# Kernel optimization log

Measured on AMD Instinct MI355X. Metric: run time of the kernel, lower is better.

## Reference

```python
import jax, jax.numpy as jnp
import numpy as np

H = 16        # num_attention_heads
G = 16        # groups
SCALE_MIN = 0.95
SCALE_MAX = 1.05


def setup_inputs() -> dict:
    key = jax.random.key(0)
    ks = jax.random.split(key, 9)
    B, S, E = 2, 2048, 1024
    d = {
        'hidden_states': jax.random.normal(ks[0], (B, S, E), jnp.float32),
        'Wq': jax.random.normal(ks[1], (E, E), jnp.float32) * (E ** -0.5),
        'bq': jax.random.normal(ks[2], (E,), jnp.float32) * 0.02,
        'Wk': jax.random.normal(ks[3], (E, E), jnp.float32) * (E ** -0.5),
        'bk': jax.random.normal(ks[4], (E,), jnp.float32) * 0.02,
        'Wv': jax.random.normal(ks[5], (E, E), jnp.float32) * (E ** -0.5),
        'bv': jax.random.normal(ks[6], (E,), jnp.float32) * 0.02,
        'Ws': jax.random.normal(ks[7], (H * G, E), jnp.float32) * (E ** -0.5),
        'bs': jax.random.normal(ks[8], (H * G,), jnp.float32) * 0.02,
    }
    return d


def _shape_heads(x, B, S):
    # [B,S,h*D] -> [B,h,S,D]
    return x.reshape(B, S, H, -1).transpose(0, 2, 1, 3)


def reference(hidden_states, Wq, bq, Wk, bk, Wv, bv, Ws, bs):
    B, S, E = hidden_states.shape
    D = E // H            # head dim = 64
    gd = D // G           # group dim = 4

    Q = _shape_heads(hidden_states @ Wq.T + bq, B, S)   # [B,h,S,D]
    K = _shape_heads(hidden_states @ Wk.T + bk, B, S)
    V = _shape_heads(hidden_states @ Wv.T + bv, B, S)

    # groupwise dynamic scales, narrow sigmoid range
    s_logits = hidden_states @ Ws.T + bs                 # [B,S,h*g]
    s = jax.nn.sigmoid(s_logits) * (SCALE_MAX - SCALE_MIN) + SCALE_MIN
    s = s.reshape(B, S, H, G).transpose(0, 2, 1, 3)      # [B,h,S,g]
    s = jnp.repeat(s, gd, axis=-1)                       # [B,h,S,D]

    Q = Q * s  # apply_to='q'

    scores = jnp.einsum('bhsd,bhtd->bhst', Q, K) / jnp.sqrt(jnp.float32(D))
    probs = jax.nn.softmax(scores, axis=-1)
    ctx = jnp.einsum('bhst,bhtd->bhsd', probs, V)        # [B,h,S,D]
    ctx = ctx.transpose(0, 2, 1, 3).reshape(B, S, H * D)
    return ctx
```

## Files before the change

kernel.cpp:

```cpp
#include <hip/hip_runtime.h>

typedef short bf16x8 __attribute__((ext_vector_type(8)));
typedef short bf16x4 __attribute__((ext_vector_type(4)));
typedef float f32x4 __attribute__((ext_vector_type(4)));

__device__ inline float bf2f(ushort u) {
    unsigned v = ((unsigned)u) << 16;
    return __builtin_bit_cast(float, v);
}
__device__ inline ushort f2bf(float f) {
    unsigned u = __builtin_bit_cast(unsigned, f);
    u += 0x7fffu + ((u >> 16) & 1u);
    return (ushort)(u >> 16);
}
__device__ inline void async_load16(const ushort* g, ushort* l) {
    __builtin_amdgcn_global_load_lds((const __attribute__((address_space(1))) void*)g,
                                     (__attribute__((address_space(3))) void*)l, 16, 0, 0);
}
__device__ inline f32x4 mfma16(bf16x4 a, bf16x4 b, f32x4 c) {
#if __has_builtin(__builtin_amdgcn_mfma_f32_16x16x16_bf16)
    return __builtin_amdgcn_mfma_f32_16x16x16_bf16(a, b, c, 0, 0, 0);
#else
    return __builtin_amdgcn_mfma_f32_16x16x16bf16_1k(a, b, c, 0, 0, 0);
#endif
}

__global__ void cast_all(const float* __restrict__ hs, const float* __restrict__ Wq,
                         const float* __restrict__ Wk, const float* __restrict__ Wv,
                         const float* __restrict__ Ws,
                         ushort* __restrict__ dhs, ushort* __restrict__ dWq,
                         ushort* __restrict__ dWk, ushort* __restrict__ dWv,
                         ushort* __restrict__ dWs)
{
    int bid = blockIdx.x;
    const float* src; ushort* dst; int off;
    if (bid < 2048)      { src = hs; dst = dhs; off = bid; }
    else if (bid < 2560) { src = Wq; dst = dWq; off = bid - 2048; }
    else if (bid < 3072) { src = Wk; dst = dWk; off = bid - 2560; }
    else if (bid < 3584) { src = Wv; dst = dWv; off = bid - 3072; }
    else                 { src = Ws; dst = dWs; off = bid - 3584; }
    int i = (off * 256 + threadIdx.x) * 8;
    float4 a = *(const float4*)(src + i);
    float4 b = *(const float4*)(src + i + 4);
    union { ushort u[8]; float4 v; } o;
    o.u[0] = f2bf(a.x); o.u[1] = f2bf(a.y); o.u[2] = f2bf(a.z); o.u[3] = f2bf(a.w);
    o.u[4] = f2bf(b.x); o.u[5] = f2bf(b.y); o.u[6] = f2bf(b.z); o.u[7] = f2bf(b.w);
    *(float4*)(dst + i) = o.v;
}

__launch_bounds__(256, 4)
__global__ void fused_qkvs(const ushort* __restrict__ X,
                           const ushort* __restrict__ Wq, const ushort* __restrict__ Wk,
                           const ushort* __restrict__ Wv, const ushort* __restrict__ Ws,
                           const float* __restrict__ bq, const float* __restrict__ bk,
                           const float* __restrict__ bv, const float* __restrict__ bs,
                           ushort* __restrict__ Qb, ushort* __restrict__ Kb,
                           ushort* __restrict__ VtG, float* __restrict__ sb)
{
    __shared__ __align__(16) ushort Sm[128 * 136];
    ushort* As = Sm;
    ushort* Bs = Sm + 128 * 64;

    const int tid = threadIdx.x, w = tid >> 6, lane = tid & 63;
    const int l15 = lane & 15, quad = lane >> 4;
    const int lrow = lane >> 3;
    const int gchunk = ((lane & 7) ^ lrow) * 8;

    const int wid = blockIdx.x;
    const int r8 = wid & 7, jj = wid >> 3;
    const int by = (jj & 3) * 8 + r8;
    const int xb = jj >> 2;
    const int m0 = by * 128;

    const ushort* W; const float* bias; int n0, mode;
    if (xb < 8)       { W = Wq; bias = bq; n0 = xb * 128;        mode = 1; }
    else if (xb < 16) { W = Wk; bias = bk; n0 = (xb - 8) * 128;  mode = 0; }
    else if (xb < 24) { W = Wv; bias = bv; n0 = (xb - 16) * 128; mode = 2; }
    else              { W = Ws; bias = bs; n0 = (xb - 24) * 128; mode = 3; }

    const int wm = (w >> 1) * 64, wn = (w & 1) * 64;

    f32x4 acc[4][4];
    for (int i = 0; i < 4; i++) for (int j = 0; j < 4; j++) acc[i][j] = (f32x4){0.f, 0.f, 0.f, 0.f};

    for (int k0 = 0; k0 < 1024; k0 += 64) {
        __syncthreads();
        for (int c = 0; c < 4; ++c) {
            int r = w * 32 + c * 8;
            async_load16(&X[(size_t)(m0 + r + lrow) * 1024 + k0 + gchunk], &As[r * 64]);
            async_load16(&W[(size_t)(n0 + r + lrow) * 1024 + k0 + gchunk], &Bs[r * 64]);
        }
        __syncthreads();
        for (int kk = 0; kk < 64; kk += 32) {
            const int csw = quad + (kk >> 3);
            bf16x8 a[4], b[4];
            for (int i = 0; i < 4; i++)
                a[i] = *(const bf16x8*)&As[(wm + i * 16 + l15) * 64 + ((csw ^ (l15 & 7)) * 8)];
            for (int j = 0; j < 4; j++)
                b[j] = *(const bf16x8*)&Bs[(wn + j * 16 + l15) * 64 + ((csw ^ (l15 & 7)) * 8)];
            for (int i = 0; i < 4; i++)
                for (int j = 0; j < 4; j++)
                    acc[i][j] = __builtin_amdgcn_mfma_f32_16x16x32_bf16(a[i], b[j], acc[i][j], 0, 0, 0);
        }
    }

    const float QSCALE = 0.125f * 1.44269504f;

    if (mode == 3) {
        for (int i = 0; i < 4; i++)
            for (int j = 0; j < 4; j++) {
                int gn = n0 + wn + j * 16 + l15;
                float bv_ = bias[gn];
                for (int r = 0; r < 4; r++) {
                    int gm = m0 + wm + i * 16 + quad * 4 + r;
                    float v = acc[i][j][r] + bv_;
                    float sg = __builtin_amdgcn_rcpf(1.0f + __builtin_amdgcn_exp2f(-v * 1.44269504f));
                    sb[(size_t)gm * 256 + gn] = sg * 0.1f + 0.95f;
                }
            }
        return;
    }

    __syncthreads();

    if (mode == 2) {
        for (int i = 0; i < 4; i++)
            for (int j = 0; j < 4; j++) {
                int gnl = wn + j * 16 + l15;
                float bv_ = bias[n0 + gnl];
                ushort4 pk;
                pk.x = f2bf(acc[i][j][0] + bv_);
                pk.y = f2bf(acc[i][j][1] + bv_);
                pk.z = f2bf(acc[i][j][2] + bv_);
                pk.w = f2bf(acc[i][j][3] + bv_);
                *(ushort4*)&Sm[gnl * 136 + wm + i * 16 + quad * 4] = pk;
            }
        __syncthreads();
        const int bb = m0 >> 11, sloc = m0 & 2047;
        for (int it = 0; it < 8; ++it) {
            int d = (tid >> 4) + it * 16;
            int s8 = (tid & 15) * 8;
            float4 v = *(float4*)&Sm[d * 136 + s8];
            int h = (n0 + d) >> 6, dd = d & 63;
            *(float4*)&VtG[(size_t)(bb * 16 + h) * 131072 + (size_t)dd * 2048 + sloc + s8] = v;
        }
    } else {
        for (int i = 0; i < 4; i++)
            for (int j = 0; j < 4; j++) {
                int gnl = wn + j * 16 + l15;
                float bv_ = bias[n0 + gnl];
                for (int r = 0; r < 4; r++) {
                    float v = acc[i][j][r] + bv_;
                    if (mode == 1) v *= QSCALE;
                    Sm[(wm + i * 16 + quad * 4 + r) * 136 + gnl] = f2bf(v);
                }
            }
        __syncthreads();
        ushort* dst = (mode == 1) ? Qb : Kb;
        for (int it = 0; it < 8; ++it) {
            int row = (tid >> 4) + it * 16, c = (tid & 15) * 8;
            *(float4*)&dst[(size_t)(m0 + row) * 1024 + n0 + c] = *(float4*)&Sm[row * 136 + c];
        }
    }
}

__launch_bounds__(256, 2)
__global__ void attn_kernel(const ushort* __restrict__ Q, const ushort* __restrict__ K,
                            const ushort* __restrict__ Vt, const float* __restrict__ sb,
                            float* __restrict__ out)
{
    __shared__ __align__(16) ushort SmA[4 * 4096 + 8192];
    ushort* Ks0 = SmA;
    ushort* Ks1 = SmA + 4096;
    ushort* Vs0 = SmA + 8192;
    ushort* Vs1 = SmA + 12288;
    ushort* Qs  = SmA + 16384;

    const int tid = threadIdx.x, w = tid >> 6, lane = tid & 63;
    const int l15 = lane & 15, quad = lane >> 4;
    const int lrow = lane >> 3;
    const int gchunk = ((lane & 7) ^ lrow) * 8;

    const int wid = blockIdx.x;
    const int r8 = wid & 7, jj = wid >> 3;
    const int bh = (jj & 3) * 8 + r8;
    const int qx = jj >> 2;
    const int b = bh >> 4, h = bh & 15;
    const int q0 = qx * 128;
    const size_t rowbase = (size_t)b * 2048;
    const int cbase = h * 64;

    const ushort* kg = K + (rowbase + w * 16 + lrow) * 1024 + cbase + gchunk;
    const ushort* vg = Vt + (size_t)bh * 131072 + (size_t)(w * 16 + lrow) * 2048 + gchunk;

    for (int c = 0; c < 2; ++c) {
        async_load16(kg + c * 8192,  Ks0 + w * 1024 + c * 512);
        async_load16(vg + c * 16384, Vs0 + w * 1024 + c * 512);
    }

    for (int it = 0; it < 4; ++it) {
        int l = tid + it * 256;
        int r = l >> 3, ch = l & 7;
        int c = ch * 8;
        union { float4 f; ushort u[8]; } uu, oo;
        uu.f = *(const float4*)&Q[(rowbase + q0 + r) * 1024 + cbase + c];
        const float* sp = &sb[(rowbase + q0 + r) * 256 + ((cbase + c) >> 2)];
        float s0 = sp[0], s1 = sp[1];
        for (int j = 0; j < 4; j++) oo.u[j] = f2bf(bf2f(uu.u[j]) * s0);
        for (int j = 4; j < 8; j++) oo.u[j] = f2bf(bf2f(uu.u[j]) * s1);
        *(float4*)&Qs[r * 64 + ((ch ^ (r & 7)) * 8)] = oo.f;
    }
    __syncthreads();

    bf16x8 aq[2][2];
    for (int mt = 0; mt < 2; mt++)
        for (int kk2 = 0; kk2 < 2; kk2++)
            aq[mt][kk2] = *(const bf16x8*)&Qs[(w * 32 + mt * 16 + l15) * 64
                                              + (((kk2 * 4 + quad) ^ (l15 & 7)) * 8)];

    int kvoff[2][4];
    for (int kk2 = 0; kk2 < 2; kk2++)
        for (int nt = 0; nt < 4; nt++)
            kvoff[kk2][nt] = (nt * 16 + l15) * 64 + (((quad + kk2 * 4) ^ (l15 & 7)) * 8);
    int vaddr[4];
    for (int kt2 = 0; kt2 < 4; kt2++)
        vaddr[kt2] = l15 * 64 + (quad & 1) * 4
                   + (((kt2 * 2 + (quad >> 1)) ^ (l15 & 7)) * 8);

    const bf16x4 vones4 = {0x3F80, 0x3F80, 0x3F80, 0x3F80};

    f32x4 osum[2];
    f32x4 o[2][4];
    for (int mt = 0; mt < 2; mt++) {
        osum[mt] = (f32x4){0.f, 0.f, 0.f, 0.f};
        for (int nt = 0; nt < 4; nt++) o[mt][nt] = (f32x4){0.f, 0.f, 0.f, 0.f};
    }
    const f32x4 z4 = (f32x4){0.f, 0.f, 0.f, 0.f};

#define ATTN_STEP(KC, VC, KN, VN, KT, PREFETCH)                                                         \
    {                                                                                                   \
        __syncthreads();                  \
        if (PREFETCH) {                                                                                 \
            const int nk = (KT) + 1;                                                                    \
            for (int c = 0; c < 2; ++c) {                                                               \
                async_load16(kg + nk * 65536 + c * 8192, KN + w * 1024 + c * 512);                      \
                async_load16(vg + nk * 64 + c * 16384,   VN + w * 1024 + c * 512);                      \
            }                                                                                           \
        }                                                                                               \
        bf16x8 kb[2][4];                                                                                \
        for (int kk2 = 0; kk2 < 2; kk2++)                                                               \
            for (int nt = 0; nt < 4; nt++)                                                              \
                kb[kk2][nt] = *(const bf16x8*)&KC[kvoff[kk2][nt]];                                      \
        bf16x4 vb4[4][4];                                                                               \
        _Pragma("unroll")                                                                               \
        for (int kt2 = 0; kt2 < 4; kt2++)                                                               \
            _Pragma("unroll")                                                                           \
            for (int nt = 0; nt < 4; nt++)                                                              \
                vb4[kt2][nt] = *(const bf16x4*)&VC[vaddr[kt2] + nt * 1024];                             \
        _Pragma("unroll")                                                                               \
        for (int mt = 0; mt < 2; mt++) {                                                                \
                                                     \
            f32x4 st[4];                                                                                \
            _Pragma("unroll")                                                                           \
            for (int kt2 = 0; kt2 < 4; kt2++) {                                                         \
                st[kt2] = __builtin_amdgcn_mfma_f32_16x16x32_bf16(kb[0][kt2], aq[mt][0], z4, 0, 0, 0);  \
                st[kt2] = __builtin_amdgcn_mfma_f32_16x16x32_bf16(kb[1][kt2], aq[mt][1], st[kt2],       \
                                                                  0, 0, 0);                             \
            }                                                                                           \
                           \
            unsigned du0[4], du1[4];                                                                    \
            _Pragma("unroll")                                                                           \
            for (int kt2 = 0; kt2 < 4; kt2++) {                                                         \
                float p0 = __builtin_amdgcn_exp2f(st[kt2][0]);                                          \
                float p1 = __builtin_amdgcn_exp2f(st[kt2][1]);                                          \
                float p2 = __builtin_amdgcn_exp2f(st[kt2][2]);                                          \
                float p3 = __builtin_amdgcn_exp2f(st[kt2][3]);                                          \
                du0[kt2] = __builtin_amdgcn_perm(__builtin_bit_cast(unsigned, p1) + 0x8000u,            \
                                                 __builtin_bit_cast(unsigned, p0) + 0x8000u,            \
                                                 0x07060302u);                                          \
                du1[kt2] = __builtin_amdgcn_perm(__builtin_bit_cast(unsigned, p3) + 0x8000u,            \
                                                 __builtin_bit_cast(unsigned, p2) + 0x8000u,            \
                                                 0x07060302u);                                          \
            }                                                                                           \
                              \
            _Pragma("unroll")                                                                           \
            for (int kt2 = 0; kt2 < 4; kt2++) {                                                         \
                union { unsigned u[2]; bf16x4 v; } af;                                                  \
                af.u[0] = du0[kt2]; af.u[1] = du1[kt2];                                                 \
                osum[mt] = mfma16(af.v, vones4, osum[mt]);                                              \
                _Pragma("unroll")                                                                       \
                for (int nt = 0; nt < 4; nt++)                                                          \
                    o[mt][nt] = mfma16(af.v, vb4[kt2][nt], o[mt][nt]);                                  \
            }                                                                                           \
        }                                                                                               \
    }

    for (int kt = 0; kt < 32; kt += 2) {
        ATTN_STEP(Ks0, Vs0, Ks1, Vs1, kt, 1);
        ATTN_STEP(Ks1, Vs1, Ks0, Vs0, kt + 1, (kt + 2 < 32));
    }
#undef ATTN_STEP

    for (int mt = 0; mt < 2; mt++) {
        for (int r = 0; r < 4; r++) {
            float iv = __builtin_amdgcn_rcpf(osum[mt][r]);
            int q = q0 + w * 32 + mt * 16 + quad * 4 + r;
            size_t base = (rowbase + q) * 1024 + cbase;
            for (int nt = 0; nt < 4; nt++)
                out[base + nt * 16 + l15] = o[mt][nt][r] * iv;
        }
    }
}

extern "C" void kernel_launch(void* const* d_in, const int* in_sizes, int n_in,
                              void* d_out, int out_size, void* d_ws, size_t ws_size,
                              hipStream_t stream) {
    const float* hs = (const float*)d_in[0];
    const float* Wq = (const float*)d_in[1];
    const float* bq = (const float*)d_in[2];
    const float* Wk = (const float*)d_in[3];
    const float* bk = (const float*)d_in[4];
    const float* Wv = (const float*)d_in[5];
    const float* bv = (const float*)d_in[6];
    const float* Ws = (const float*)d_in[7];
    const float* bs = (const float*)d_in[8];
    float* outp = (float*)d_out;

    char* ws = (char*)d_ws;
    ushort* Qb    = (ushort*)(ws);
    ushort* Kb    = (ushort*)(ws + 8388608);
    ushort* VtG   = (ushort*)(ws + 16777216);
    float*  sb    = (float* )(ws + 25165824);
    ushort* hs_bf = (ushort*)(ws + 29360128);
    ushort* Wq_bf = (ushort*)(ws + 37748736);
    ushort* Wk_bf = (ushort*)(ws + 39845888);
    ushort* Wv_bf = (ushort*)(ws + 41943040);
    ushort* Ws_bf = (ushort*)(ws + 44040192);

    cast_all<<<dim3(3712), dim3(256), 0, stream>>>(hs, Wq, Wk, Wv, Ws,
                                                   hs_bf, Wq_bf, Wk_bf, Wv_bf, Ws_bf);
    fused_qkvs<<<dim3(832), dim3(256), 0, stream>>>(hs_bf, Wq_bf, Wk_bf, Wv_bf, Ws_bf,
                                                    bq, bk, bv, bs, Qb, Kb, VtG, sb);
    attn_kernel<<<dim3(512), dim3(256), 0, stream>>>(Qb, Kb, VtG, sb, outp);
}
```

Before: 169.3 us.

## Double KV tile size per barrier and load scaled Q directly to registers

```diff
diff --git a/kernel.cpp b/kernel.cpp
--- a/kernel.cpp
+++ b/kernel.cpp
@@ -169,12 +169,11 @@
                             const ushort* __restrict__ Vt, const float* __restrict__ sb,
                             float* __restrict__ out)
 {
-    __shared__ __align__(16) ushort SmA[4 * 4096 + 8192];
+    __shared__ __align__(16) ushort SmA[4 * 8192];
     ushort* Ks0 = SmA;
-    ushort* Ks1 = SmA + 4096;
-    ushort* Vs0 = SmA + 8192;
-    ushort* Vs1 = SmA + 12288;
-    ushort* Qs  = SmA + 16384;
+    ushort* Ks1 = SmA + 8192;
+    ushort* Vs0 = SmA + 16384;
+    ushort* Vs1 = SmA + 24576;
 
     const int tid = threadIdx.x, w = tid >> 6, lane = tid & 63;
     const int l15 = lane & 15, quad = lane >> 4;
@@ -190,33 +189,29 @@
     const size_t rowbase = (size_t)b * 2048;
     const int cbase = h * 64;
 
-    const ushort* kg = K + (rowbase + w * 16 + lrow) * 1024 + cbase + gchunk;
+    const ushort* kg = K + (rowbase + w * 32 + lrow) * 1024 + cbase + gchunk;
     const ushort* vg = Vt + (size_t)bh * 131072 + (size_t)(w * 16 + lrow) * 2048 + gchunk;
 
-    for (int c = 0; c < 2; ++c) {
-        async_load16(kg + c * 8192,  Ks0 + w * 1024 + c * 512);
-        async_load16(vg + c * 16384, Vs0 + w * 1024 + c * 512);
-    }
-
-    for (int it = 0; it < 4; ++it) {
-        int l = tid + it * 256;
-        int r = l >> 3, ch = l & 7;
-        int c = ch * 8;
-        union { float4 f; ushort u[8]; } uu, oo;
-        uu.f = *(const float4*)&Q[(rowbase + q0 + r) * 1024 + cbase + c];
-        const float* sp = &sb[(rowbase + q0 + r) * 256 + ((cbase + c) >> 2)];
-        float s0 = sp[0], s1 = sp[1];
-        for (int j = 0; j < 4; j++) oo.u[j] = f2bf(bf2f(uu.u[j]) * s0);
-        for (int j = 4; j < 8; j++) oo.u[j] = f2bf(bf2f(uu.u[j]) * s1);
-        *(float4*)&Qs[r * 64 + ((ch ^ (r & 7)) * 8)] = oo.f;
-    }
-    __syncthreads();
+    for (int c = 0; c < 4; ++c)
+        async_load16(kg + c * 8192, Ks0 + w * 2048 + c * 512);
+    for (int ss = 0; ss < 2; ++ss)
+        for (int c = 0; c < 2; ++c)
+            async_load16(vg + ss * 64 + c * 16384, Vs0 + ss * 4096 + w * 1024 + c * 512);
 
     bf16x8 aq[2][2];
     for (int mt = 0; mt < 2; mt++)
-        for (int kk2 = 0; kk2 < 2; kk2++)
-            aq[mt][kk2] = *(const bf16x8*)&Qs[(w * 32 + mt * 16 + l15) * 64
-                                              + (((kk2 * 4 + quad) ^ (l15 & 7)) * 8)];
+        for (int kk2 = 0; kk2 < 2; kk2++) {
+            size_t qrow = rowbase + q0 + w * 32 + mt * 16 + l15;
+            int c0 = cbase + kk2 * 32 + quad * 8;
+            union { float4 f; ushort u[8]; } uu;
+            union { ushort u[8]; bf16x8 v; } oo;
+            uu.f = *(const float4*)&Q[qrow * 1024 + c0];
+            const float* sp = &sb[qrow * 256 + (c0 >> 2)];
+            float s0 = sp[0], s1 = sp[1];
+            for (int j = 0; j < 4; j++) oo.u[j] = f2bf(bf2f(uu.u[j]) * s0);
+            for (int j = 4; j < 8; j++) oo.u[j] = f2bf(bf2f(uu.u[j]) * s1);
+            aq[mt][kk2] = oo.v;
+        }
 
     int kvoff[2][4];
     for (int kk2 = 0; kk2 < 2; kk2++)
@@ -242,62 +237,70 @@
         __syncthreads();                  \
         if (PREFETCH) {                                                                                 \
             const int nk = (KT) + 1;                                                                    \
-            for (int c = 0; c < 2; ++c) {                                                               \
-                async_load16(kg + nk * 65536 + c * 8192, KN + w * 1024 + c * 512);                      \
-                async_load16(vg + nk * 64 + c * 16384,   VN + w * 1024 + c * 512);                      \
+            for (int c = 0; c < 4; ++c)                                                                 \
+                async_load16(kg + (size_t)nk * 131072 + c * 8192, KN + w * 2048 + c * 512);             \
+            for (int ss = 0; ss < 2; ++ss)                                                              \
+                for (int c = 0; c < 2; ++c)                                                             \
+                    async_load16(vg + nk * 128 + ss * 64 + c * 16384,                                   \
+                                 VN + ss * 4096 + w * 1024 + c * 512);                                  \
+        }                                                                                               \
+        _Pragma("unroll")                                                                               \
+        for (int sub = 0; sub < 2; ++sub) {                                                             \
+            const ushort* KCs = KC + sub * 4096;                                                        \
+            const ushort* VCs = VC + sub * 4096;                                                        \
+            bf16x8 kb[2][4];                                                                            \
+            for (int kk2 = 0; kk2 < 2; kk2++)                                                           \
+                for (int nt = 0; nt < 4; nt++)                                                          \
+                    kb[kk2][nt] = *(const bf16x8*)&KCs[kvoff[kk2][nt]];                                 \
+            bf16x4 vb4[4][4];                                                                           \
+            _Pragma("unroll")                                                                           \
+            for (int kt2 = 0; kt2 < 4; kt2++)                                                           \
+                _Pragma("unroll")                                                                       \
+                for (int nt = 0; nt < 4; nt++)                                                          \
+                    vb4[kt2][nt] = *(const bf16x4*)&VCs[vaddr[kt2] + nt * 1024];                        \
+            _Pragma("unroll")                                                                           \
+            for (int mt = 0; mt < 2; mt++) {                                                            \
+                                                     \
+                f32x4 st[4];                                                                            \
+                _Pragma("unroll")                                                                       \
+                for (int kt2 = 0; kt2 < 4; kt2++) {                                                     \
+                    st[kt2] = __builtin_amdgcn_mfma_f32_16x16x32_bf16(kb[0][kt2], aq[mt][0],            \
+                                                                      z4, 0, 0, 0);                     \
+                    st[kt2] = __builtin_amdgcn_mfma_f32_16x16x32_bf16(kb[1][kt2], aq[mt][1],            \
+                                                                      st[kt2], 0, 0, 0);                \
+                }                                                                                       \
+                           \
+                unsigned du0[4], du1[4];                                                                \
+                _Pragma("unroll")                                                                       \
+                for (int kt2 = 0; kt2 < 4; kt2++) {                                                     \
+                    float p0 = __builtin_amdgcn_exp2f(st[kt2][0]);                                      \
+                    float p1 = __builtin_amdgcn_exp2f(st[kt2][1]);                                      \
+                    float p2 = __builtin_amdgcn_exp2f(st[kt2][2]);                                      \
+                    float p3 = __builtin_amdgcn_exp2f(st[kt2][3]);                                      \
+                    du0[kt2] = __builtin_amdgcn_perm(__builtin_bit_cast(unsigned, p1) + 0x8000u,        \
+                                                     __builtin_bit_cast(unsigned, p0) + 0x8000u,        \
+                                                     0x07060302u);                                      \
+                    du1[kt2] = __builtin_amdgcn_perm(__builtin_bit_cast(unsigned, p3) + 0x8000u,        \
+                                                     __builtin_bit_cast(unsigned, p2) + 0x8000u,        \
+                                                     0x07060302u);                                      \
+                }                                                                                       \
+                              \
+                _Pragma("unroll")                                                                       \
+                for (int kt2 = 0; kt2 < 4; kt2++) {                                                     \
+                    union { unsigned u[2]; bf16x4 v; } af;                                              \
+                    af.u[0] = du0[kt2]; af.u[1] = du1[kt2];                                             \
+                    osum[mt] = mfma16(af.v, vones4, osum[mt]);                                          \
+                    _Pragma("unroll")                                                                   \
+                    for (int nt = 0; nt < 4; nt++)                                                      \
+                        o[mt][nt] = mfma16(af.v, vb4[kt2][nt], o[mt][nt]);                              \
+                }                                                                                       \
             }                                                                                           \
         }                                                                                               \
-        bf16x8 kb[2][4];                                                                                \
-        for (int kk2 = 0; kk2 < 2; kk2++)                                                               \
-            for (int nt = 0; nt < 4; nt++)                                                              \
-                kb[kk2][nt] = *(const bf16x8*)&KC[kvoff[kk2][nt]];                                      \
-        bf16x4 vb4[4][4];                                                                               \
-        _Pragma("unroll")                                                                               \
-        for (int kt2 = 0; kt2 < 4; kt2++)                                                               \
-            _Pragma("unroll")                                                                           \
-            for (int nt = 0; nt < 4; nt++)                                                              \
-                vb4[kt2][nt] = *(const bf16x4*)&VC[vaddr[kt2] + nt * 1024];                             \
-        _Pragma("unroll")                                                                               \
-        for (int mt = 0; mt < 2; mt++) {                                                                \
-                                                     \
-            f32x4 st[4];                                                                                \
-            _Pragma("unroll")                                                                           \
-            for (int kt2 = 0; kt2 < 4; kt2++) {                                                         \
-                st[kt2] = __builtin_amdgcn_mfma_f32_16x16x32_bf16(kb[0][kt2], aq[mt][0], z4, 0, 0, 0);  \
-                st[kt2] = __builtin_amdgcn_mfma_f32_16x16x32_bf16(kb[1][kt2], aq[mt][1], st[kt2],       \
-                                                                  0, 0, 0);                             \
-            }                                                                                           \
-                           \
-            unsigned du0[4], du1[4];                                                                    \
-            _Pragma("unroll")                                                                           \
-            for (int kt2 = 0; kt2 < 4; kt2++) {                                                         \
-                float p0 = __builtin_amdgcn_exp2f(st[kt2][0]);                                          \
-                float p1 = __builtin_amdgcn_exp2f(st[kt2][1]);                                          \
-                float p2 = __builtin_amdgcn_exp2f(st[kt2][2]);                                          \
-                float p3 = __builtin_amdgcn_exp2f(st[kt2][3]);                                          \
-                du0[kt2] = __builtin_amdgcn_perm(__builtin_bit_cast(unsigned, p1) + 0x8000u,            \
-                                                 __builtin_bit_cast(unsigned, p0) + 0x8000u,            \
-                                                 0x07060302u);                                          \
-                du1[kt2] = __builtin_amdgcn_perm(__builtin_bit_cast(unsigned, p3) + 0x8000u,            \
-                                                 __builtin_bit_cast(unsigned, p2) + 0x8000u,            \
-                                                 0x07060302u);                                          \
-            }                                                                                           \
-                              \
-            _Pragma("unroll")                                                                           \
-            for (int kt2 = 0; kt2 < 4; kt2++) {                                                         \
-                union { unsigned u[2]; bf16x4 v; } af;                                                  \
-                af.u[0] = du0[kt2]; af.u[1] = du1[kt2];                                                 \
-                osum[mt] = mfma16(af.v, vones4, osum[mt]);                                              \
-                _Pragma("unroll")                                                                       \
-                for (int nt = 0; nt < 4; nt++)                                                          \
-                    o[mt][nt] = mfma16(af.v, vb4[kt2][nt], o[mt][nt]);                                  \
-            }                                                                                           \
-        }                                                                                               \
-    }
-
-    for (int kt = 0; kt < 32; kt += 2) {
+    }
+
+    for (int kt = 0; kt < 16; kt += 2) {
         ATTN_STEP(Ks0, Vs0, Ks1, Vs1, kt, 1);
-        ATTN_STEP(Ks1, Vs1, Ks0, Vs0, kt + 1, (kt + 2 < 32));
+        ATTN_STEP(Ks1, Vs1, Ks0, Vs0, kt + 1, (kt + 2 < 16));
     }
 #undef ATTN_STEP
 
```

After: 170.0 us. Within noise of the previous version (+0.4%).
